# Kernel tuning notes

Measured on AMD Instinct MI355X. Metric: run time of the kernel, lower is better.

## Reference

```python
import jax, jax.numpy as jnp
import numpy as np

# Single LSTM cell step from ZERO initial state (h0=c0=0), vectorized over (B,T).
# PyTorch gate order: i, f, g, o. Since h0=0 the W_hh contribution is exactly 0
# and since c0=0 the forget-gate term vanishes: c = sigmoid(i)*tanh(g).

def _cell(inp, W_ih, b_ih, b_hh):
    # inp: (B,T,in), W_ih: (4H,in) -> gates (B,T,4H)
    g = jnp.einsum('bti,gi->btg', inp, W_ih) + b_ih + b_hh
    i_, f_, g_, o_ = jnp.split(g, 4, axis=-1)
    c = jax.nn.sigmoid(i_) * jnp.tanh(g_)
    h = jax.nn.sigmoid(o_) * jnp.tanh(c)
    return h, c


def setup_inputs() -> dict:
    key = jax.random.key(0)
    ks = jax.random.split(key, 11)
    B, T, E, H, V = 32, 256, 512, 512, 50000
    s = 1.0 / np.sqrt(H)  # keep gates out of deep saturation
    return {
        'x': jax.random.randint(ks[0], (B, T), 0, V, dtype=jnp.int32),
        'emb': jax.random.normal(ks[1], (V, E), jnp.float32),
        'W_ih_l0': jax.random.normal(ks[2], (2, 4 * H, E), jnp.float32) * s,
        'W_hh_l0': jax.random.normal(ks[3], (2, 4 * H, H), jnp.float32) * s,
        'b_ih_l0': jax.random.normal(ks[4], (2, 4 * H), jnp.float32) * s,
        'b_hh_l0': jax.random.normal(ks[5], (2, 4 * H), jnp.float32) * s,
        'W_ih_l1': jax.random.normal(ks[6], (2, 4 * H, 2 * H), jnp.float32) * s,
        'W_hh_l1': jax.random.normal(ks[7], (2, 4 * H, H), jnp.float32) * s,
        'b_ih_l1': jax.random.normal(ks[8], (2, 4 * H), jnp.float32) * s,
        'b_hh_l1': jax.random.normal(ks[9], (2, 4 * H), jnp.float32) * s,
    }


def reference(x, emb, W_ih_l0, W_hh_l0, b_ih_l0, b_hh_l0,
              W_ih_l1, W_hh_l1, b_ih_l1, b_hh_l1):
    e = emb[x]  # (B,T,E)
    # layer 0, forward/backward directions (seq_len==1 per step, so both
    # directions see the same token from zero state, with separate weights)
    h0f, c0f = _cell(e, W_ih_l0[0], b_ih_l0[0], b_hh_l0[0])
    h0b, c0b = _cell(e, W_ih_l0[1], b_ih_l0[1], b_hh_l0[1])
    inp1 = jnp.concatenate([h0f, h0b], axis=-1)  # (B,T,2H)
    h1f, c1f = _cell(inp1, W_ih_l1[0], b_ih_l1[0], b_hh_l1[0])
    h1b, c1b = _cell(inp1, W_ih_l1[1], b_ih_l1[1], b_hh_l1[1])
    # encoder_out: per-timestep h_n summed over directions -> (B,T,L,H)
    encoder_out = jnp.stack([h0f + h0b, h1f + h1b], axis=2)
    # h_last: forward-direction h_n and c_n at last timestep -> (L,B,H)
    h_last = jnp.stack([h0f[:, -1], h1f[:, -1]], axis=0)
    c_last = jnp.stack([c0f[:, -1], c1f[:, -1]], axis=0)
    return h_last, c_last, encoder_out
```

## Files before the change

kernel.cpp:

```cpp
#include <hip/hip_runtime.h>
#include <hip/hip_bf16.h>


using bf16x8 = __attribute__((ext_vector_type(8))) short;
using f32x4  = __attribute__((ext_vector_type(4))) float;

__device__ __forceinline__ unsigned short f2bf(float f)
{
    __hip_bfloat16 h = __float2bfloat16(f);
    return *(unsigned short*)&h;
}
__device__ __forceinline__ float sigf(float x)  { return 1.0f / (1.0f + __expf(-x)); }
__device__ __forceinline__ float tanhfast(float x)
{
    return 1.0f - 2.0f / (__expf(2.0f * x) + 1.0f);
}

__device__ __forceinline__ void gload16(const void* g, void* l)
{
    __builtin_amdgcn_global_load_lds(
        (const __attribute__((address_space(1))) unsigned int*)g,
        (__attribute__((address_space(3))) unsigned int*)l, 16, 0, 0);
}

__global__ __launch_bounds__(256)
void prep(const int* __restrict__ x, const void* __restrict__ emb,
          const void* __restrict__ Wih0, const void* __restrict__ Wih1,
          const void* __restrict__ bih0, const void* __restrict__ bhh0,
          const void* __restrict__ bih1, const void* __restrict__ bhh1,
          uint4* __restrict__ e0, uint4* __restrict__ Wp0, uint4* __restrict__ Wp1,
          float* __restrict__ bc0, float* __restrict__ bc1, int* __restrict__ flag)
{
    __shared__ int oks[4];
    {
        unsigned lo = ((const unsigned int*)emb)[threadIdx.x] & 0xFFFFu;
        int e = (lo >> 7) & 0xFF;
        int ok = ((e >= 96 && e < 160) || lo == 0) ? 1 : 0;
#pragma unroll
        for (int off = 32; off; off >>= 1) ok += __shfl_down(ok, off);
        if ((threadIdx.x & 63) == 0) oks[threadIdx.x >> 6] = ok;
    }
    __syncthreads();
    const bool isbf = (oks[0] + oks[1] + oks[2] + oks[3]) >= 192;
    const int bid = blockIdx.x, tid = threadIdx.x;

    if (bid < 2048) {
        int idx = bid * 256 + tid;
        int m = idx >> 6, r = idx & 63;
        long srow = x[m];
        uint4 v;
        if (isbf) {
            v = ((const uint4*)emb)[srow * 64 + r];
        } else {
            const float4* ef = (const float4*)emb;
            float4 a = ef[srow * 128 + r * 2], b = ef[srow * 128 + r * 2 + 1];
            unsigned short h[8] = { f2bf(a.x), f2bf(a.y), f2bf(a.z), f2bf(a.w),
                                    f2bf(b.x), f2bf(b.y), f2bf(b.z), f2bf(b.w) };
            v = *(uint4*)h;
        }
        e0[idx] = v;
    } else if (bid < 4352) {
        const bool L0 = bid < 2816;
        const int  ks = L0 ? 6 : 7;
        int idx = (L0 ? (bid - 2048) : (bid - 2816)) * 256 + tid;
        const void* src = L0 ? Wih0 : Wih1;
        uint4* dst = L0 ? Wp0 : Wp1;
        int n = idx >> ks, r = idx & ((1 << ks) - 1);
        int h = n / 6, gi = n % 6;
        int dir = (gi >= 3) ? 1 : 0;
        int gate = gi - dir * 3;
        int sg = (gate == 0) ? 0 : (gate + 1);
        long c8 = ((long)(dir * 2048 + sg * 512 + h) << ks) + r;
        if (isbf) {
            dst[idx] = ((const uint4*)src)[c8];
        } else {
            const float4* sf = (const float4*)src;
            float4 a = sf[c8 * 2], b = sf[c8 * 2 + 1];
            unsigned short h8[8] = { f2bf(a.x), f2bf(a.y), f2bf(a.z), f2bf(a.w),
                                     f2bf(b.x), f2bf(b.y), f2bf(b.z), f2bf(b.w) };
            dst[idx] = *(uint4*)h8;
        }
    } else {
        int b2 = bid - 4352;
        if (b2 == 0 && tid == 0) *flag = isbf ? 1 : 0;
        const bool L0 = b2 < 12;
        int n = (L0 ? b2 : (b2 - 12)) * 256 + tid;
        int h = n / 6, gi = n % 6;
        int dir = (gi >= 3) ? 1 : 0;
        int gate = gi - dir * 3;
        int sg = (gate == 0) ? 0 : (gate + 1);
        int s = dir * 2048 + sg * 512 + h;
        const void* bi = L0 ? bih0 : bih1;
        const void* bh = L0 ? bhh0 : bhh1;
        float* bc = L0 ? bc0 : bc1;
        float vi, vh;
        if (isbf) {
            vi = __bfloat162float(((const __hip_bfloat16*)bi)[s]);
            vh = __bfloat162float(((const __hip_bfloat16*)bh)[s]);
        } else {
            vi = ((const float*)bi)[s];
            vh = ((const float*)bh)[s];
        }
        bc[n] = vi + vh;
    }
}

template <int LAYER>
__global__ __launch_bounds__(512)
void gemm_fused(const unsigned short* __restrict__ A,
                const unsigned short* __restrict__ Bp,
                const float* __restrict__ bc,
                unsigned short* __restrict__ inp1,
                void* __restrict__ outv,
                const int* __restrict__ flag,
                int K)
{
    constexpr int BM = 256, BN = 96, BK = 32;
    __shared__ __align__(16) char smem[45056];

    const int tid = threadIdx.x, bm = blockIdx.x, bn = blockIdx.y;
    const int K8 = K >> 3;
    const uint4* a4 = (const uint4*)A;
    const uint4* b4 = (const uint4*)Bp;

    const long aBase0 = (long)(bm * BM + (tid >> 2)) * K8 + (tid & 3);
    const long aBase1 = aBase0 + (long)128 * K8;
    const long bBase0 = (long)(bn * BN + (tid >> 2)) * K8 + (tid & 3);
    const bool bact = tid < 384;

    const int wave = tid >> 6, lane = tid & 63;
    const int wr = (wave >> 1) * 64;
    const int wc = (wave & 1) * 48;
    const int lr = lane & 15, q = lane >> 4;

    f32x4 acc[4][3] = {};
    const int NT = K / BK;

    auto stage = [&](int buf, int k8) {
        uint4* As4 = (uint4*)(smem + buf * 16384);
        uint4* Bs4 = (uint4*)(smem + 32768 + buf * 6144);
        gload16(a4 + aBase0 + k8, As4 + tid);
        gload16(a4 + aBase1 + k8, As4 + tid + 512);
        if (bact) gload16(b4 + bBase0 + k8, Bs4 + tid);
    };

    stage(0, 0);
    __syncthreads();
    for (int t = 0; t < NT; ++t) {
        if (t + 1 < NT) stage((t + 1) & 1, (t + 1) * (BK >> 3));
        const unsigned short* As = (const unsigned short*)(smem + (t & 1) * 16384);
        const unsigned short* Bs = (const unsigned short*)(smem + 32768 + (t & 1) * 6144);
        bf16x8 af[4], bf[3];
#pragma unroll
        for (int i = 0; i < 4; ++i)
            af[i] = *(const bf16x8*)&As[(wr + i * 16 + lr) * BK + q * 8];
#pragma unroll
        for (int j = 0; j < 3; ++j)
            bf[j] = *(const bf16x8*)&Bs[(wc + j * 16 + lr) * BK + q * 8];
#pragma unroll
        for (int i = 0; i < 4; ++i)
#pragma unroll
            for (int j = 0; j < 3; ++j)
                acc[i][j] = __builtin_amdgcn_mfma_f32_16x16x32_bf16(af[i], bf[j], acc[i][j], 0, 0, 0);
        __syncthreads();
    }

    float* Cs = (float*)smem;
    const bool isbf = (*flag != 0);
    auto store = [&](long i, float v) {
        if (isbf) ((__hip_bfloat16*)outv)[i] = __float2bfloat16(v);
        else      ((float*)outv)[i] = v;
    };

    const int hl = tid & 15;
    float bcv[6];
#pragma unroll
    for (int gi = 0; gi < 6; ++gi) bcv[gi] = bc[bn * BN + hl * 6 + gi];

    for (int p = 0; p < 4; ++p) {
        if ((wave >> 1) == p) {
#pragma unroll
            for (int i = 0; i < 4; ++i)
#pragma unroll
                for (int j = 0; j < 3; ++j)
#pragma unroll
                    for (int r = 0; r < 4; ++r)
                        Cs[(i * 16 + q * 4 + r) * 97 + wc + j * 16 + lr] = acc[i][j][r];
        }
        __syncthreads();
#pragma unroll
        for (int t2 = 0; t2 < 2; ++t2) {
            int ml = (tid >> 4) + t2 * 32;
            float z[6];
#pragma unroll
            for (int gi = 0; gi < 6; ++gi) z[gi] = Cs[ml * 97 + hl * 6 + gi] + bcv[gi];
            float c0 = sigf(z[0]) * tanhfast(z[1]);
            float h0 = sigf(z[2]) * tanhfast(c0);
            float c1 = sigf(z[3]) * tanhfast(z[4]);
            float h1 = sigf(z[5]) * tanhfast(c1);

            long m = (long)bm * BM + p * 64 + ml;
            int hg = bn * 16 + hl;

            if constexpr (LAYER == 0) {
                inp1[m * 1024 + hg]       = f2bf(h0);
                inp1[m * 1024 + 512 + hg] = f2bf(h1);
            }
            store(65536 + m * 1024 + LAYER * 512 + hg, h0 + h1);
            if ((m & 255) == 255) {
                int b = (int)(m >> 8);
                store(LAYER * 16384 + b * 512 + hg, h0);
                store(32768 + LAYER * 16384 + b * 512 + hg, c0);
            }
        }
        if (p < 3) __syncthreads();
    }
}

extern "C" void kernel_launch(void* const* d_in, const int* in_sizes, int n_in,
                              void* d_out, int out_size, void* d_ws, size_t ws_size,
                              hipStream_t stream)
{
    const int* x      = (const int*)d_in[0];
    const void* emb   = d_in[1];
    const void* Wih0  = d_in[2];
    const void* bih0  = d_in[4];
    const void* bhh0  = d_in[5];
    const void* Wih1  = d_in[6];
    const void* bih1  = d_in[8];
    const void* bhh1  = d_in[9];

    char* ws = (char*)d_ws;
    int*   flag           = (int*)(ws);
    float* bc0            = (float*)(ws + 1024);
    float* bc1            = (float*)(ws + 16384);
    unsigned short* Wp0   = (unsigned short*)(ws + 32768);
    unsigned short* Wp1   = (unsigned short*)(ws + 4194304);
    unsigned short* e0    = (unsigned short*)(ws + 10485760);
    unsigned short* inp1  = (unsigned short*)(ws + 18874368);

    prep<<<4376, 256, 0, stream>>>(x, emb, Wih0, Wih1, bih0, bhh0, bih1, bhh1,
                                   (uint4*)e0, (uint4*)Wp0, (uint4*)Wp1, bc0, bc1, flag);

    gemm_fused<0><<<dim3(32, 32), 512, 0, stream>>>(e0, Wp0, bc0, inp1, d_out, flag, 512);
    gemm_fused<1><<<dim3(32, 32), 512, 0, stream>>>(inp1, Wp1, bc1, nullptr, d_out, flag, 1024);
}
```

Measured before the change: 298.1 us.

## Use K-chunk-major operand layout, XCD-aware block swizzle, and finer waitcnt pipelining

Stores the embedding, the packed weights and the layer-1 input in a K8-chunk-major layout ([k8][row][8]), so each 16-byte LDS fill is a contiguous run across rows and fragment reads use a new indexing. Block ids are remapped so that blocks sharing an A tile land on the same XCD, which should improve L2 reuse. The pipeline swaps __syncthreads for explicit vmcnt waits plus raw barriers, removes the prologue sync, raises wave priority around the MFMAs, and gives inactive threads a dummy load so vmcnt counts stay uniform. The swizzle hardcodes a 32x32 grid, and the dummy load adds a small amount of redundant traffic.

```diff
diff --git a/kernel.cpp b/kernel.cpp
--- a/kernel.cpp
+++ b/kernel.cpp
@@ -22,6 +22,9 @@
         (const __attribute__((address_space(1))) unsigned int*)g,
         (__attribute__((address_space(3))) unsigned int*)l, 16, 0, 0);
 }
+#define SBAR() do { __builtin_amdgcn_sched_barrier(0); \
+                    __builtin_amdgcn_s_barrier();      \
+                    __builtin_amdgcn_sched_barrier(0); } while (0)
 
 __global__ __launch_bounds__(256)
 void prep(const int* __restrict__ x, const void* __restrict__ emb,
@@ -46,14 +49,14 @@
 
     if (bid < 2048) {
         int idx = bid * 256 + tid;
-        int m = idx >> 6, r = idx & 63;
+        int k8 = idx >> 13, m = idx & 8191;
         long srow = x[m];
         uint4 v;
         if (isbf) {
-            v = ((const uint4*)emb)[srow * 64 + r];
+            v = ((const uint4*)emb)[srow * 64 + k8];
         } else {
             const float4* ef = (const float4*)emb;
-            float4 a = ef[srow * 128 + r * 2], b = ef[srow * 128 + r * 2 + 1];
+            float4 a = ef[srow * 128 + k8 * 2], b = ef[srow * 128 + k8 * 2 + 1];
             unsigned short h[8] = { f2bf(a.x), f2bf(a.y), f2bf(a.z), f2bf(a.w),
                                     f2bf(b.x), f2bf(b.y), f2bf(b.z), f2bf(b.w) };
             v = *(uint4*)h;
@@ -61,21 +64,21 @@
         e0[idx] = v;
     } else if (bid < 4352) {
         const bool L0 = bid < 2816;
-        const int  ks = L0 ? 6 : 7;
         int idx = (L0 ? (bid - 2048) : (bid - 2816)) * 256 + tid;
-        const void* src = L0 ? Wih0 : Wih1;
-        uint4* dst = L0 ? Wp0 : Wp1;
-        int n = idx >> ks, r = idx & ((1 << ks) - 1);
-        int h = n / 6, gi = n % 6;
+        int k8 = idx / 3072, n = idx - k8 * 3072;
+        int h = n / 6, gi = n - h * 6;
         int dir = (gi >= 3) ? 1 : 0;
         int gate = gi - dir * 3;
         int sg = (gate == 0) ? 0 : (gate + 1);
-        long c8 = ((long)(dir * 2048 + sg * 512 + h) << ks) + r;
+        long srcrow = dir * 2048 + sg * 512 + h;
+        const void* src = L0 ? Wih0 : Wih1;
+        uint4* dst = L0 ? Wp0 : Wp1;
+        const int K4 = L0 ? 128 : 256, K8 = L0 ? 64 : 128;
         if (isbf) {
-            dst[idx] = ((const uint4*)src)[c8];
+            dst[idx] = ((const uint4*)src)[srcrow * K8 + k8];
         } else {
             const float4* sf = (const float4*)src;
-            float4 a = sf[c8 * 2], b = sf[c8 * 2 + 1];
+            float4 a = sf[srcrow * K4 + k8 * 2], b = sf[srcrow * K4 + k8 * 2 + 1];
             unsigned short h8[8] = { f2bf(a.x), f2bf(a.y), f2bf(a.z), f2bf(a.w),
                                      f2bf(b.x), f2bf(b.y), f2bf(b.z), f2bf(b.w) };
             dst[idx] = *(uint4*)h8;
@@ -85,7 +88,7 @@
         if (b2 == 0 && tid == 0) *flag = isbf ? 1 : 0;
         const bool L0 = b2 < 12;
         int n = (L0 ? b2 : (b2 - 12)) * 256 + tid;
-        int h = n / 6, gi = n % 6;
+        int h = n / 6, gi = n - h * 6;
         int dir = (gi >= 3) ? 1 : 0;
         int gate = gi - dir * 3;
         int sg = (gate == 0) ? 0 : (gate + 1);
@@ -115,17 +118,21 @@
                 const int* __restrict__ flag,
                 int K)
 {
-    constexpr int BM = 256, BN = 96, BK = 32;
-    __shared__ __align__(16) char smem[45056];
-
-    const int tid = threadIdx.x, bm = blockIdx.x, bn = blockIdx.y;
-    const int K8 = K >> 3;
+    __shared__ __align__(16) char smem[45072];
+
+    const int tid = threadIdx.x;
+    const int raw = blockIdx.x + (blockIdx.y << 5);
+    const int xcd = raw & 7, local = raw >> 3;
+    const int bm = xcd * 4 + (local >> 5);
+    const int bn = local & 31;
+
     const uint4* a4 = (const uint4*)A;
     const uint4* b4 = (const uint4*)Bp;
 
-    const long aBase0 = (long)(bm * BM + (tid >> 2)) * K8 + (tid & 3);
-    const long aBase1 = aBase0 + (long)128 * K8;
-    const long bBase0 = (long)(bn * BN + (tid >> 2)) * K8 + (tid & 3);
+    const int aRow = bm * 256 + (tid & 255);
+    const int aK   = tid >> 8;
+    const int bK   = (tid < 384) ? (tid / 96) : 0;
+    const int bN   = bn * 96 + ((tid < 384) ? (tid - (tid / 96) * 96) : 0);
     const bool bact = tid < 384;
 
     const int wave = tid >> 6, lane = tid & 63;
@@ -134,35 +141,47 @@
     const int lr = lane & 15, q = lane >> 4;
 
     f32x4 acc[4][3] = {};
-    const int NT = K / BK;
-
-    auto stage = [&](int buf, int k8) {
+    const int NT = K >> 5;
+
+    auto stage = [&](int t) {
+        const int buf = t & 1;
+        const int k8b = t * 4;
         uint4* As4 = (uint4*)(smem + buf * 16384);
         uint4* Bs4 = (uint4*)(smem + 32768 + buf * 6144);
-        gload16(a4 + aBase0 + k8, As4 + tid);
-        gload16(a4 + aBase1 + k8, As4 + tid + 512);
-        if (bact) gload16(b4 + bBase0 + k8, Bs4 + tid);
+        const uint4* s0 = a4 + (long)(k8b + aK) * 8192 + aRow;
+        gload16(s0, As4 + tid);
+        gload16(s0 + 2L * 8192, As4 + tid + 512);
+        if (bact) gload16(b4 + (long)(k8b + bK) * 3072 + bN, Bs4 + tid);
+        else      gload16(s0, (uint4*)(smem + 45056));
     };
 
-    stage(0, 0);
-    __syncthreads();
+    stage(0);
     for (int t = 0; t < NT; ++t) {
-        if (t + 1 < NT) stage((t + 1) & 1, (t + 1) * (BK >> 3));
+        if (t + 1 < NT) {
+            stage(t + 1);
+            asm volatile("s_waitcnt vmcnt(3)" ::: "memory");
+        } else {
+            asm volatile("s_waitcnt vmcnt(0)" ::: "memory");
+        }
+        SBAR();
+
         const unsigned short* As = (const unsigned short*)(smem + (t & 1) * 16384);
         const unsigned short* Bs = (const unsigned short*)(smem + 32768 + (t & 1) * 6144);
         bf16x8 af[4], bf[3];
 #pragma unroll
         for (int i = 0; i < 4; ++i)
-            af[i] = *(const bf16x8*)&As[(wr + i * 16 + lr) * BK + q * 8];
+            af[i] = *(const bf16x8*)&As[(q * 256 + wr + i * 16 + lr) * 8];
 #pragma unroll
         for (int j = 0; j < 3; ++j)
-            bf[j] = *(const bf16x8*)&Bs[(wc + j * 16 + lr) * BK + q * 8];
+            bf[j] = *(const bf16x8*)&Bs[(q * 96 + wc + j * 16 + lr) * 8];
+        __builtin_amdgcn_s_setprio(1);
 #pragma unroll
         for (int i = 0; i < 4; ++i)
 #pragma unroll
             for (int j = 0; j < 3; ++j)
                 acc[i][j] = __builtin_amdgcn_mfma_f32_16x16x32_bf16(af[i], bf[j], acc[i][j], 0, 0, 0);
-        __syncthreads();
+        __builtin_amdgcn_s_setprio(0);
+        SBAR();
     }
 
     float* Cs = (float*)smem;
@@ -175,7 +194,7 @@
     const int hl = tid & 15;
     float bcv[6];
 #pragma unroll
-    for (int gi = 0; gi < 6; ++gi) bcv[gi] = bc[bn * BN + hl * 6 + gi];
+    for (int gi = 0; gi < 6; ++gi) bcv[gi] = bc[bn * 96 + hl * 6 + gi];
 
     for (int p = 0; p < 4; ++p) {
         if ((wave >> 1) == p) {
@@ -199,12 +218,13 @@
             float c1 = sigf(z[3]) * tanhfast(z[4]);
             float h1 = sigf(z[5]) * tanhfast(c1);
 
-            long m = (long)bm * BM + p * 64 + ml;
+            long m = (long)bm * 256 + p * 64 + ml;
             int hg = bn * 16 + hl;
 
             if constexpr (LAYER == 0) {
-                inp1[m * 1024 + hg]       = f2bf(h0);
-                inp1[m * 1024 + 512 + hg] = f2bf(h1);
+                int c0i = hg, c1i = 512 + hg;
+                inp1[((long)(c0i >> 3) * 8192 + m) * 8 + (c0i & 7)] = f2bf(h0);
+                inp1[((long)(c1i >> 3) * 8192 + m) * 8 + (c1i & 7)] = f2bf(h1);
             }
             store(65536 + m * 1024 + LAYER * 512 + hg, h0 + h1);
             if ((m & 255) == 255) {
```

Result: no change. 295.1 us (-1.0%).
